# Optimization experiments

Hardware: AMD Instinct MI355X
Metric: run time of the kernel (lower is better)

Reference implementation:

```python
import jax, jax.numpy as jnp
import numpy as np

WINDOW_SIZE = 11
SIGMA = 1.5
C1 = 0.01 ** 2
C2 = 0.03 ** 2


def _gaussian_window(channels):
    # 1D gaussian, normalized, then outer product -> (C,1,K,K) depthwise kernel
    coords = np.arange(WINDOW_SIZE, dtype=np.float32) - WINDOW_SIZE // 2
    g = np.exp(-(coords ** 2) / (2.0 * SIGMA ** 2))
    g = g / g.sum()
    w2d = np.outer(g, g).astype(np.float32)  # (K,K)
    w = np.broadcast_to(w2d, (channels, 1, WINDOW_SIZE, WINDOW_SIZE))
    return jnp.asarray(w)


def _dw_conv(x, w):
    # depthwise conv, SAME-style padding = K//2 (matches conv2d(padding=K//2, groups=C))
    pad = WINDOW_SIZE // 2
    return jax.lax.conv_general_dilated(
        x, w,
        window_strides=(1, 1),
        padding=[(pad, pad), (pad, pad)],
        dimension_numbers=("NCHW", "OIHW", "NCHW"),
        feature_group_count=x.shape[1],
    )


def _ssim(img1, img2):
    w = _gaussian_window(img1.shape[1]).astype(img1.dtype)
    mu1 = _dw_conv(img1, w)
    mu2 = _dw_conv(img2, w)
    mu1_sq = mu1 * mu1
    mu2_sq = mu2 * mu2
    mu1_mu2 = mu1 * mu2
    sigma1_sq = _dw_conv(img1 * img1, w) - mu1_sq
    sigma2_sq = _dw_conv(img2 * img2, w) - mu2_sq
    sigma12 = _dw_conv(img1 * img2, w) - mu1_mu2
    ssim_map = ((2.0 * mu1_mu2 + C1) * (2.0 * sigma12 + C2)) / (
        (mu1_sq + mu2_sq + C1) * (sigma1_sq + sigma2_sq + C2)
    )
    return jnp.mean(ssim_map)


def setup_inputs() -> dict:
    key = jax.random.key(0)
    k1, k2 = jax.random.split(key)
    shape = (16, 3, 512, 512)
    r_low = jax.random.uniform(k1, shape, dtype=jnp.float32)
    r_high = jax.random.uniform(k2, shape, dtype=jnp.float32)
    return {"r_low": r_low, "r_high": r_high}


def reference(r_low, r_high):
    ssim_loss = 1.0 - _ssim(r_low, r_high)
    mse_loss = jnp.mean((r_low - r_high) ** 2)
    return ssim_loss + mse_loss
```

## Files before the change

### kernel.cpp

```cpp
#include <hip/hip_runtime.h>
#include <cmath>


#define HH 512
#define WW 512
#define TILE_H 32
#define TILE_W 64
#define HB (TILE_H + 10)
#define LDW 65
#define NPLANES 48
#define CT (WW / TILE_W)
#define RT (HH / TILE_H)
#define NBLOCKS (NPLANES * RT * CT)

struct GW { float g[11]; };

__global__ __launch_bounds__(256, 3)
void ssim_main(const float* __restrict__ img1, const float* __restrict__ img2,
               float* __restrict__ partial, GW gw)
{
    __shared__ float4 hbuf[HB][LDW];
    __shared__ float red[4];

    const int tid   = threadIdx.x;
    const int bx    = blockIdx.x;
    const int by    = blockIdx.y;
    const int plane = blockIdx.z;
    const int row0  = by * TILE_H;
    const int col0  = bx * TILE_W;
    const float* p1 = img1 + (size_t)plane * (HH * WW);
    const float* p2 = img2 + (size_t)plane * (HH * WW);

    const int cg    = tid & 15;
    const int rs    = tid >> 4;
    const int cbase = col0 + 4 * cg - 8;

    auto loadRow = [&](int grow, float4* x1, float4* x2) {
        const int growc = min(max(grow, 0), HH - 1);
        const float* r1 = p1 + (size_t)growc * WW;
        const float* r2 = p2 + (size_t)growc * WW;
        #pragma unroll
        for (int v = 0; v < 5; ++v) {
            const int c0 = cbase + 4 * v;
            if (c0 >= 0 && c0 + 4 <= WW) {
                x1[v] = *reinterpret_cast<const float4*>(r1 + c0);
                x2[v] = *reinterpret_cast<const float4*>(r2 + c0);
            } else {
                x1[v] = make_float4(0.f, 0.f, 0.f, 0.f);
                x2[v] = make_float4(0.f, 0.f, 0.f, 0.f);
            }
        }
    };

    auto convStore = [&](int rl, const float4* x1v, const float4* x2v) {
        const int   grow  = row0 - 5 + rl;
        const float rmask = (grow >= 0 && grow < HH) ? 1.f : 0.f;
        const float* x1 = reinterpret_cast<const float*>(x1v);
        const float* x2 = reinterpret_cast<const float*>(x2v);
        float acc[4][4];
        #pragma unroll
        for (int k = 0; k < 4; ++k)
            #pragma unroll
            for (int i = 0; i < 4; ++i) acc[k][i] = 0.f;
        #pragma unroll
        for (int e = 3; e <= 16; ++e) {
            float a  = x1[e], b = x2[e];
            float v2 = a * a + b * b;
            float v3 = a * b;
            #pragma unroll
            for (int i = 0; i < 4; ++i) {
                int j = e - 3 - i;
                if (j >= 0 && j < 11) {
                    float w = gw.g[j];
                    acc[0][i] += w * a;
                    acc[1][i] += w * b;
                    acc[2][i] += w * v2;
                    acc[3][i] += w * v3;
                }
            }
        }
        #pragma unroll
        for (int i = 0; i < 4; ++i)
            hbuf[rl][4 * cg + i] =
                make_float4(acc[0][i] * rmask, acc[1][i] * rmask,
                            acc[2][i] * rmask, acc[3][i] * rmask);
    };

    {
        float4 xA1[5], xA2[5], xB1[5], xB2[5];
        const bool third = (rs < 10);
        loadRow(row0 - 5 + rs, xA1, xA2);
        loadRow(row0 + 11 + rs, xB1, xB2);
        convStore(rs, xA1, xA2);
        if (third) loadRow(row0 + 27 + rs, xA1, xA2);
        convStore(rs + 16, xB1, xB2);
        if (third) convStore(rs + 32, xA1, xA2);
    }

    const int tx = tid & 63;
    const int rg = tid >> 6;
    float mse_a[8], mse_b[8];
    #pragma unroll
    for (int p = 0; p < 8; ++p) {
        size_t off = (size_t)(row0 + rg * 8 + p) * WW + col0 + tx;
        mse_a[p] = p1[off];
        mse_b[p] = p2[off];
    }
    __syncthreads();

    float local = 0.f;
    {
        float4 res[8];
        #pragma unroll
        for (int p = 0; p < 8; ++p) res[p] = make_float4(0.f, 0.f, 0.f, 0.f);
        #pragma unroll
        for (int j = 0; j < 18; ++j) {
            float4 w4 = hbuf[rg * 8 + j][tx];
            #pragma unroll
            for (int p = 0; p < 8; ++p) {
                int t = j - p;
                if (t >= 0 && t < 11) {
                    float w = gw.g[t];
                    res[p].x += w * w4.x;
                    res[p].y += w * w4.y;
                    res[p].z += w * w4.z;
                    res[p].w += w * w4.w;
                }
            }
        }
        const float C1c = 0.0001f, C2c = 0.0009f;
        #pragma unroll
        for (int p = 0; p < 8; ++p) {
            float mu1 = res[p].x, mu2 = res[p].y;
            float S   = res[p].z, P   = res[p].w;
            float m11 = mu1 * mu1, m22 = mu2 * mu2, m12 = mu1 * mu2;
            float num = (2.f * m12 + C1c) * (2.f * (P - m12) + C2c);
            float den = (m11 + m22 + C1c) * ((S - m11 - m22) + C2c);
            float inv = __builtin_amdgcn_rcpf(den);
            float d   = mse_a[p] - mse_b[p];
            local += d * d - num * inv;
        }
    }

    #pragma unroll
    for (int off = 32; off > 0; off >>= 1) local += __shfl_down(local, off);
    if ((tid & 63) == 0) red[tid >> 6] = local;
    __syncthreads();
    if (tid == 0) {
        int bid = (plane * RT + by) * CT + bx;
        partial[bid] = (red[0] + red[1]) + (red[2] + red[3]);
    }
}

__global__ __launch_bounds__(256)
void ssim_finish(const float* __restrict__ partial, float* __restrict__ out)
{
    __shared__ float red[256];
    float s = 0.f;
    #pragma unroll
    for (int i = 0; i < NBLOCKS / 256; ++i)
        s += partial[i * 256 + threadIdx.x];
    red[threadIdx.x] = s;
    __syncthreads();
    for (int step = 128; step > 0; step >>= 1) {
        if ((int)threadIdx.x < step) red[threadIdx.x] += red[threadIdx.x + step];
        __syncthreads();
    }
    if (threadIdx.x == 0)
        out[0] = 1.0f + red[0] * (1.0f / 12582912.0f);
}

extern "C" void kernel_launch(void* const* d_in, const int* in_sizes, int n_in,
                              void* d_out, int out_size, void* d_ws, size_t ws_size,
                              hipStream_t stream)
{
    const float* r_low  = (const float*)d_in[0];
    const float* r_high = (const float*)d_in[1];
    float* out     = (float*)d_out;
    float* partial = (float*)d_ws;

    GW gw;
    {
        float s = 0.f;
        for (int i = 0; i < 11; ++i) {
            float c = (float)(i - 5);
            gw.g[i] = expf(-(c * c) / 4.5f);
            s += gw.g[i];
        }
        for (int i = 0; i < 11; ++i) gw.g[i] /= s;
    }

    dim3 grid(CT, RT, NPLANES);
    ssim_main<<<grid, dim3(256), 0, stream>>>(r_low, r_high, partial, gw);
    ssim_finish<<<1, dim3(256), 0, stream>>>(partial, out);
}
```

Before: 172.9 us.

## Switch to tall 64x32 tiles, vectorize MSE loads, mask rows at load time

Changes the block tile from 32x64 to 64x32, so vertical halo overhead drops from 10/32 to 10/64 rows while horizontal halo grows. Thread mapping for horizontal pass and MSE loads is reworked: MSE reads use float4 loads and rows outside the image are zeroed at load instead of masked after convolution. Occupancy hint is raised to 4 blocks per SM. This trades more horizontal halo loads and narrower 128-byte row segments for less vertical redundancy, and the smaller shared buffer permits higher occupancy.

New measurement: 171.8 us. No clear change (-0.6%).

```diff
diff --git a/kernel.cpp b/kernel.cpp
--- a/kernel.cpp
+++ b/kernel.cpp
@@ -4,10 +4,10 @@
 
 #define HH 512
 #define WW 512
-#define TILE_H 32
-#define TILE_W 64
+#define TILE_H 64
+#define TILE_W 32
 #define HB (TILE_H + 10)
-#define LDW 65
+#define LDW 33
 #define NPLANES 48
 #define CT (WW / TILE_W)
 #define RT (HH / TILE_H)
@@ -15,7 +15,7 @@
 
 struct GW { float g[11]; };
 
-__global__ __launch_bounds__(256, 3)
+__global__ __launch_bounds__(256, 4)
 void ssim_main(const float* __restrict__ img1, const float* __restrict__ img2,
                float* __restrict__ partial, GW gw)
 {
@@ -31,18 +31,19 @@
     const float* p1 = img1 + (size_t)plane * (HH * WW);
     const float* p2 = img2 + (size_t)plane * (HH * WW);
 
-    const int cg    = tid & 15;
-    const int rs    = tid >> 4;
+    const int cg    = tid & 7;
+    const int rs    = tid >> 3;
     const int cbase = col0 + 4 * cg - 8;
 
     auto loadRow = [&](int grow, float4* x1, float4* x2) {
+        const bool rowOK = (grow >= 0 && grow < HH);
         const int growc = min(max(grow, 0), HH - 1);
         const float* r1 = p1 + (size_t)growc * WW;
         const float* r2 = p2 + (size_t)growc * WW;
         #pragma unroll
         for (int v = 0; v < 5; ++v) {
             const int c0 = cbase + 4 * v;
-            if (c0 >= 0 && c0 + 4 <= WW) {
+            if (rowOK && c0 >= 0 && c0 + 4 <= WW) {
                 x1[v] = *reinterpret_cast<const float4*>(r1 + c0);
                 x2[v] = *reinterpret_cast<const float4*>(r2 + c0);
             } else {
@@ -53,8 +54,6 @@
     };
 
     auto convStore = [&](int rl, const float4* x1v, const float4* x2v) {
-        const int   grow  = row0 - 5 + rl;
-        const float rmask = (grow >= 0 && grow < HH) ? 1.f : 0.f;
         const float* x1 = reinterpret_cast<const float*>(x1v);
         const float* x2 = reinterpret_cast<const float*>(x2v);
         float acc[4][4];
@@ -82,34 +81,35 @@
         #pragma unroll
         for (int i = 0; i < 4; ++i)
             hbuf[rl][4 * cg + i] =
-                make_float4(acc[0][i] * rmask, acc[1][i] * rmask,
-                            acc[2][i] * rmask, acc[3][i] * rmask);
+                make_float4(acc[0][i], acc[1][i], acc[2][i], acc[3][i]);
     };
 
     {
         float4 xA1[5], xA2[5], xB1[5], xB2[5];
         const bool third = (rs < 10);
         loadRow(row0 - 5 + rs, xA1, xA2);
-        loadRow(row0 + 11 + rs, xB1, xB2);
+        loadRow(row0 + 27 + rs, xB1, xB2);
         convStore(rs, xA1, xA2);
-        if (third) loadRow(row0 + 27 + rs, xA1, xA2);
-        convStore(rs + 16, xB1, xB2);
-        if (third) convStore(rs + 32, xA1, xA2);
-    }
-
-    const int tx = tid & 63;
-    const int rg = tid >> 6;
-    float mse_a[8], mse_b[8];
+        if (third) loadRow(row0 + 59 + rs, xA1, xA2);
+        convStore(rs + 32, xB1, xB2);
+        if (third) convStore(rs + 64, xA1, xA2);
+    }
+
+    const int mc = (tid & 7) * 4;
+    const int mr = tid >> 3;
+    float4 mse_a[2], mse_b[2];
     #pragma unroll
-    for (int p = 0; p < 8; ++p) {
-        size_t off = (size_t)(row0 + rg * 8 + p) * WW + col0 + tx;
-        mse_a[p] = p1[off];
-        mse_b[p] = p2[off];
+    for (int q = 0; q < 2; ++q) {
+        size_t off = (size_t)(row0 + 2 * mr + q) * WW + col0 + mc;
+        mse_a[q] = *reinterpret_cast<const float4*>(p1 + off);
+        mse_b[q] = *reinterpret_cast<const float4*>(p2 + off);
     }
     __syncthreads();
 
     float local = 0.f;
     {
+        const int tx = tid & 31;
+        const int rg = tid >> 5;
         float4 res[8];
         #pragma unroll
         for (int p = 0; p < 8; ++p) res[p] = make_float4(0.f, 0.f, 0.f, 0.f);
@@ -137,8 +137,15 @@
             float num = (2.f * m12 + C1c) * (2.f * (P - m12) + C2c);
             float den = (m11 + m22 + C1c) * ((S - m11 - m22) + C2c);
             float inv = __builtin_amdgcn_rcpf(den);
-            float d   = mse_a[p] - mse_b[p];
-            local += d * d - num * inv;
+            local -= num * inv;
+        }
+        #pragma unroll
+        for (int q = 0; q < 2; ++q) {
+            float dx = mse_a[q].x - mse_b[q].x;
+            float dy = mse_a[q].y - mse_b[q].y;
+            float dz = mse_a[q].z - mse_b[q].z;
+            float dw = mse_a[q].w - mse_b[q].w;
+            local += dx * dx + dy * dy + dz * dz + dw * dw;
         }
     }
 
```
